# Kernel optimization log

Hardware: AMD Instinct MI355X
Metric: run time of the kernel (lower is better)

The kernel has to match this reference:

```python
import jax, jax.numpy as jnp
import numpy as np

EMBED = 4096
HEADS = 16
HEAD_DIM = EMBED // HEADS  # 256
ROT = 64                   # rotary_dim
B, S = 1, 2048
MASK_VAL = -1.0e9          # masked_bias


def setup_inputs() -> dict:
    key = jax.random.key(0)
    ks = jax.random.split(key, 5)
    sc = 0.02
    return {
        "hidden_states": jax.random.normal(ks[0], (B, S, EMBED), jnp.float32),
        "Wq": jax.random.normal(ks[1], (EMBED, EMBED), jnp.float32) * sc,
        "Wk": jax.random.normal(ks[2], (EMBED, EMBED), jnp.float32) * sc,
        "Wv": jax.random.normal(ks[3], (EMBED, EMBED), jnp.float32) * sc,
        "Wo": jax.random.normal(ks[4], (EMBED, EMBED), jnp.float32) * sc,
    }


def _rotate_every_two(x):
    # interleave: (x0,x1,x2,x3,...) -> (x1,x0,x3,x2,...)  [as written in source]
    r = jnp.stack((x[..., 1::2], x[..., ::2]), axis=-1)
    return r.reshape(x.shape)


def _fixed_pos_embedding(seq_len, rot_dim):
    inv_freq = 1.0 / (10000.0 ** (jnp.arange(0, rot_dim, 2, dtype=jnp.float32) / rot_dim))
    t = jnp.arange(seq_len, dtype=jnp.float32)
    sinusoid = jnp.einsum('i,j->ij', t, inv_freq)  # [S, rot_dim/2]
    return jnp.sin(sinusoid), jnp.cos(sinusoid)


def _apply_rotary(x, sin, cos):
    # x: [B, S, H, ROT]; sin/cos: [S, ROT/2] -> repeat each freq twice along last dim
    sin = jnp.repeat(sin[None, :, None, :], 2, axis=3)
    cos = jnp.repeat(cos[None, :, None, :], 2, axis=3)
    return x * cos + _rotate_every_two(x) * sin


def reference(hidden_states, Wq, Wk, Wv, Wo):
    b, s, e = hidden_states.shape
    q = (hidden_states @ Wq).reshape(b, s, HEADS, HEAD_DIM)
    k = (hidden_states @ Wk).reshape(b, s, HEADS, HEAD_DIM)
    v = (hidden_states @ Wv).reshape(b, s, HEADS, HEAD_DIM)

    sin, cos = _fixed_pos_embedding(s, ROT)
    q = jnp.concatenate([_apply_rotary(q[..., :ROT], sin, cos), q[..., ROT:]], axis=-1)
    k = jnp.concatenate([_apply_rotary(k[..., :ROT], sin, cos), k[..., ROT:]], axis=-1)

    q = q.transpose(0, 2, 1, 3)  # [B,H,S,D]
    k = k.transpose(0, 2, 1, 3)
    v = v.transpose(0, 2, 1, 3)

    logits = jnp.einsum('bhqd,bhkd->bhqk', q, k)  # [B,H,S,S]
    causal = jnp.tril(jnp.ones((s, s), dtype=bool))[None, None]
    # GPT-J quirk: mask applied BEFORE scaling
    logits = jnp.where(causal, logits, MASK_VAL)
    logits = logits / jnp.sqrt(jnp.float32(HEAD_DIM))
    attn = jax.nn.softmax(logits, axis=-1)

    out = jnp.einsum('bhqk,bhkd->bhqd', attn, v)
    out = out.transpose(0, 2, 1, 3).reshape(b, s, e)
    return out @ Wo
```

## Files before the change

kernel.cpp:

```cpp
#include <hip/hip_runtime.h>
#include <hip/hip_bf16.h>
#include <math.h>

#define EMBED 4096
#define SLEN 2048
#define HEADS 16
#define HDIM 256
#define ROT 64

typedef __bf16 bf16;
typedef __attribute__((ext_vector_type(8))) __bf16 bf16x8;
typedef __attribute__((ext_vector_type(4))) float f32x4;

__device__ __forceinline__ void async_copy16(const void* g, void* l) {
  __builtin_amdgcn_global_load_lds((const __attribute__((address_space(1))) void*)g,
                                   (__attribute__((address_space(3))) void*)l,
                                   16, 0, 0);
}

__global__ __launch_bounds__(256) void cast_kernel(const float* __restrict__ in,
                                                   bf16* __restrict__ out, int n4) {
  int i = blockIdx.x * 256 + threadIdx.x;
  if (i >= n4) return;
  float4 v = ((const float4*)in)[i];
  bf16 o[4] __attribute__((aligned(8)));
  o[0] = (bf16)v.x; o[1] = (bf16)v.y; o[2] = (bf16)v.z; o[3] = (bf16)v.w;
  ((ushort4*)out)[i] = *(const ushort4*)o;
}

__global__ __launch_bounds__(256) void transpose_cast(const float* __restrict__ W,
                                                      bf16* __restrict__ Wt) {
  __shared__ bf16 tile[64][65];
  int k0 = blockIdx.y * 64, n0 = blockIdx.x * 64;
  int tr = threadIdx.x >> 4, tc = threadIdx.x & 15;
#pragma unroll
  for (int i = 0; i < 4; i++) {
    int row = tr + i * 16;
    float4 v = *(const float4*)(W + (size_t)(k0 + row) * EMBED + n0 + tc * 4);
    tile[row][tc * 4 + 0] = (bf16)v.x;
    tile[row][tc * 4 + 1] = (bf16)v.y;
    tile[row][tc * 4 + 2] = (bf16)v.z;
    tile[row][tc * 4 + 3] = (bf16)v.w;
  }
  __syncthreads();
#pragma unroll
  for (int i = 0; i < 4; i++) {
    int nl = tr + i * 16;
    bf16 o[4] __attribute__((aligned(8)));
#pragma unroll
    for (int j = 0; j < 4; j++) o[j] = tile[tc * 4 + j][nl];
    *(ushort4*)(Wt + (size_t)(n0 + nl) * EMBED + k0 + tc * 4) = *(const ushort4*)o;
  }
}

template <int MODE>
__global__ __launch_bounds__(512, 1) void gemm_pipe(const bf16* __restrict__ A,
                                                    const bf16* __restrict__ Bt,
                                                    void* __restrict__ Cout,
                                                    int M, int N, int K) {
  constexpr int BM = 128, BN = 256, BK = 64;
  __shared__ __align__(16) bf16 As[3][BM * BK];
  __shared__ __align__(16) bf16 Bs[3][BN * BK];
  int t = threadIdx.x;
  int lane = t & 63, w = t >> 6;
  int c16 = lane & 15, g4 = lane >> 4;
  int wm = w >> 2, wn = w & 3;
  int m0 = blockIdx.y * BM, n0 = blockIdx.x * BN;
  int nt = K / BK;

  f32x4 acc[4][4] = {};

  auto stage = [&](int kt, int slot) {
    const bf16* Asrc = A + (size_t)m0 * K + kt * BK;
    const bf16* Bsrc = Bt + (size_t)n0 * K + kt * BK;
    bf16* Ad = As[slot];
    bf16* Bd = Bs[slot];
#pragma unroll
    for (int i = 0; i < 2; i++) {
      int c = i * 512 + t;
      int row = c >> 3, col8 = c & 7;
      async_copy16(Asrc + (size_t)row * K + ((col8 ^ (row & 7)) * 8), Ad + c * 8);
    }
#pragma unroll
    for (int i = 0; i < 4; i++) {
      int c = i * 512 + t;
      int row = c >> 3, col8 = c & 7;
      async_copy16(Bsrc + (size_t)row * K + ((col8 ^ (row & 7)) * 8), Bd + c * 8);
    }
  };

  stage(0, 0);
  stage(1, 1);
  asm volatile("s_waitcnt vmcnt(6)" ::: "memory");
  __builtin_amdgcn_s_barrier();

  for (int kt = 0; kt < nt; kt++) {
    int slot = kt - (kt / 3) * 3;
    const bf16* Ab = As[slot];
    const bf16* Bb = Bs[slot];

    bf16x8 af[2][4], bfr[2][4];
#pragma unroll
    for (int kk = 0; kk < 2; kk++) {
#pragma unroll
      for (int fm = 0; fm < 4; fm++) {
        int row = wm * 64 + fm * 16 + c16;
        af[kk][fm] = *(const bf16x8*)(Ab + row * BK + (((kk * 4 + g4) ^ (row & 7)) * 8));
      }
#pragma unroll
      for (int fn = 0; fn < 4; fn++) {
        int row = wn * 64 + fn * 16 + c16;
        bfr[kk][fn] = *(const bf16x8*)(Bb + row * BK + (((kk * 4 + g4) ^ (row & 7)) * 8));
      }
    }
    if (kt + 2 < nt) {
      int s2 = (kt + 2) - ((kt + 2) / 3) * 3;
      stage(kt + 2, s2);
    }
    __builtin_amdgcn_s_setprio(1);
#pragma unroll
    for (int kk = 0; kk < 2; kk++)
#pragma unroll
      for (int fm = 0; fm < 4; fm++)
#pragma unroll
        for (int fn = 0; fn < 4; fn++)
          acc[fm][fn] = __builtin_amdgcn_mfma_f32_16x16x32_bf16(af[kk][fm], bfr[kk][fn],
                                                                acc[fm][fn], 0, 0, 0);
    __builtin_amdgcn_s_setprio(0);
    if (kt < nt - 2) {
      asm volatile("s_waitcnt vmcnt(6)" ::: "memory");
      __builtin_amdgcn_s_barrier();
    } else if (kt == nt - 2) {
      asm volatile("s_waitcnt vmcnt(0)" ::: "memory");
      __builtin_amdgcn_s_barrier();
    }
  }

#pragma unroll
  for (int fm = 0; fm < 4; fm++) {
#pragma unroll
    for (int fn = 0; fn < 4; fn++) {
      int col = n0 + wn * 64 + fn * 16 + c16;
#pragma unroll
      for (int r = 0; r < 4; r++) {
        int row = m0 + wm * 64 + fm * 16 + g4 * 4 + r;
        float v = acc[fm][fn][r];
        if (MODE == 1) {
          int d = col & (HDIM - 1);
          if (d < ROT) {
            float pv = __shfl_xor(v, 1);
            int jj = d >> 1;
            float invf = __expf(-0.28782313662425575f * (float)jj);
            float ang = (float)row * invf;
            float sa, ca;
            sincosf(ang, &sa, &ca);
            v = v * ca + pv * sa;
          }
        }
        if (MODE == 3) {
          ((float*)Cout)[(size_t)row * N + col] = v;
        } else if (MODE == 2) {
          ((bf16*)Cout)[(size_t)col * M + row] = (bf16)v;
        } else {
          ((bf16*)Cout)[(size_t)row * N + col] = (bf16)v;
        }
      }
    }
  }
}

__global__ __launch_bounds__(256, 1) void attn_kernel(const bf16* __restrict__ Q,
                                                      const bf16* __restrict__ Kmat,
                                                      const bf16* __restrict__ Vt,
                                                      bf16* __restrict__ O) {
  __shared__ __align__(16) bf16 Ks[2][64 * 256];
  __shared__ __align__(16) bf16 Vs[2][64 * 256];
  __shared__ __align__(16) bf16 Pl[4][16 * 64];
  int t = threadIdx.x, lane = t & 63, w = t >> 6;
  int c16 = lane & 15, g4 = lane >> 4;
  int b = blockIdx.x;
  int h = (b & 7) * 2 + ((b >> 3) & 1);
  int pair = b >> 4;

  for (int pass = 0; pass < 2; ++pass) {
    int qt = pass ? (31 - pair) : pair;
    int q0w = qt * 64 + w * 16;

    bf16x8 qf[8];
    {
      const bf16* qp = Q + (size_t)(q0w + c16) * EMBED + h * HDIM + g4 * 8;
#pragma unroll
      for (int kk = 0; kk < 8; kk++) qf[kk] = *(const bf16x8*)(qp + kk * 32);
    }
    f32x4 acco[16] = {};
    float mrow[4], lrow[4];
#pragma unroll
    for (int r = 0; r < 4; r++) { mrow[r] = -1e30f; lrow[r] = 0.f; }

    __syncthreads();
#pragma unroll
    for (int j = 0; j < 8; j++) {
      int c = j * 256 + w * 64 + lane;
      int row = c >> 5, col8 = c & 31;
      int scol = (col8 ^ (row & 7)) * 8;
      async_copy16(Kmat + (size_t)(0 * 64 + row) * EMBED + h * HDIM + scol,
                   Ks[0] + (size_t)c * 8);
    }
#pragma unroll
    for (int j = 0; j < 8; j++) {
      int c = j * 256 + w * 64 + lane;
      int row = c >> 3, col8 = c & 7;
      int scol = (col8 ^ (row & 7)) * 8;
      async_copy16(Vt + (size_t)(h * HDIM + row) * SLEN + 0 * 64 + scol,
                   Vs[0] + (size_t)c * 8);
    }
    __syncthreads();

    for (int kt = 0; kt <= qt; kt++) {
      int cur = kt & 1;
      if (kt < qt) {
#pragma unroll
        for (int j = 0; j < 8; j++) {
          int c = j * 256 + w * 64 + lane;
          int row = c >> 5, col8 = c & 31;
          int scol = (col8 ^ (row & 7)) * 8;
          async_copy16(Kmat + (size_t)((kt + 1) * 64 + row) * EMBED + h * HDIM + scol,
                       Ks[cur ^ 1] + (size_t)c * 8);
        }
#pragma unroll
        for (int j = 0; j < 8; j++) {
          int c = j * 256 + w * 64 + lane;
          int row = c >> 3, col8 = c & 7;
          int scol = (col8 ^ (row & 7)) * 8;
          async_copy16(Vt + (size_t)(h * HDIM + row) * SLEN + (kt + 1) * 64 + scol,
                       Vs[cur ^ 1] + (size_t)c * 8);
        }
      }
      const bf16* KsB = Ks[cur];
      const bf16* VsB = Vs[cur];

      f32x4 accs[4] = {};
      __builtin_amdgcn_s_setprio(1);
#pragma unroll
      for (int kk = 0; kk < 8; kk++) {
#pragma unroll
        for (int fn = 0; fn < 4; fn++) {
          int r = fn * 16 + c16;
          bf16x8 kf = *(const bf16x8*)(KsB + r * 256 + ((kk * 4 + g4) ^ (c16 & 7)) * 8);
          accs[fn] = __builtin_amdgcn_mfma_f32_16x16x32_bf16(qf[kk], kf, accs[fn], 0, 0, 0);
        }
      }
      __builtin_amdgcn_s_setprio(0);

      float pm[4][4];
      bool diag = (kt == qt);
#pragma unroll
      for (int fn = 0; fn < 4; fn++)
#pragma unroll
        for (int r = 0; r < 4; r++) {
          float s = accs[fn][r] * 0.0625f;
          if (diag) {
            int kg = fn * 16 + c16;
            int qg = w * 16 + g4 * 4 + r;
            if (kg > qg) s = -1e30f;
          }
          pm[fn][r] = s;
        }
      float lmax[4];
#pragma unroll
      for (int r = 0; r < 4; r++)
        lmax[r] = fmaxf(fmaxf(pm[0][r], pm[1][r]), fmaxf(pm[2][r], pm[3][r]));
      bool need = false;
#pragma unroll
      for (int r = 0; r < 4; r++) need = need || (lmax[r] > mrow[r] + 8.0f);
      if (__any(need)) {
#pragma unroll
        for (int r = 0; r < 4; r++) {
          float mx = lmax[r];
#pragma unroll
          for (int off = 1; off < 16; off <<= 1) mx = fmaxf(mx, __shfl_xor(mx, off));
          float mn = fmaxf(mrow[r], mx);
          float sc = __expf(mrow[r] - mn);
          mrow[r] = mn;
          lrow[r] *= sc;
#pragma unroll
          for (int fd = 0; fd < 16; fd++) acco[fd][r] *= sc;
        }
      }
#pragma unroll
      for (int fn = 0; fn < 4; fn++)
#pragma unroll
        for (int r = 0; r < 4; r++) {
          float p = __expf(pm[fn][r] - mrow[r]);
          pm[fn][r] = p;
          lrow[r] += p;
        }
#pragma unroll
      for (int fn = 0; fn < 4; fn++)
#pragma unroll
        for (int r = 0; r < 4; r++) {
          int q = g4 * 4 + r;
          int chunk = (fn * 2 + (c16 >> 3)) ^ (q & 7);
          Pl[w][q * 64 + chunk * 8 + (c16 & 7)] = (bf16)pm[fn][r];
        }
      __builtin_amdgcn_s_setprio(1);
#pragma unroll
      for (int kk2 = 0; kk2 < 2; kk2++) {
        bf16x8 pf = *(const bf16x8*)(&Pl[w][c16 * 64 + ((kk2 * 4 + g4) ^ (c16 & 7)) * 8]);
#pragma unroll
        for (int fd = 0; fd < 16; fd++) {
          int rv = fd * 16 + c16;
          bf16x8 vf = *(const bf16x8*)(VsB + rv * 64 + ((kk2 * 4 + g4) ^ (c16 & 7)) * 8);
          acco[fd] = __builtin_amdgcn_mfma_f32_16x16x32_bf16(pf, vf, acco[fd], 0, 0, 0);
        }
      }
      __builtin_amdgcn_s_setprio(0);
      __syncthreads();
    }
    float inv[4];
#pragma unroll
    for (int r = 0; r < 4; r++) {
      float s = lrow[r];
#pragma unroll
      for (int off = 1; off < 16; off <<= 1) s += __shfl_xor(s, off);
      inv[r] = 1.0f / s;
    }
#pragma unroll
    for (int fd = 0; fd < 16; fd++)
#pragma unroll
      for (int r = 0; r < 4; r++) {
        int qg = q0w + g4 * 4 + r;
        int col = h * HDIM + fd * 16 + c16;
        O[(size_t)qg * EMBED + col] = (bf16)(acco[fd][r] * inv[r]);
      }
  }
}

extern "C" void kernel_launch(void* const* d_in, const int* in_sizes, int n_in,
                              void* d_out, int out_size, void* d_ws, size_t ws_size,
                              hipStream_t stream) {
  const float* hidden = (const float*)d_in[0];
  const float* Wq = (const float*)d_in[1];
  const float* Wk = (const float*)d_in[2];
  const float* Wv = (const float*)d_in[3];
  const float* Wo = (const float*)d_in[4];
  float* out = (float*)d_out;

  char* ws = (char*)d_ws;
  const size_t SZ_H = (size_t)SLEN * EMBED * 2;
  const size_t SZ_W = (size_t)EMBED * EMBED * 2;
  if (ws_size < 5 * SZ_H + SZ_W) return;

  bf16* h_bf = (bf16*)ws;
  bf16* Wt   = (bf16*)(ws + SZ_H);
  bf16* Qb   = (bf16*)(ws + SZ_H + SZ_W);
  bf16* Kb   = (bf16*)(ws + 2 * SZ_H + SZ_W);
  bf16* Vtb  = (bf16*)(ws + 3 * SZ_H + SZ_W);
  bf16* Ob   = (bf16*)(ws + 4 * SZ_H + SZ_W);

  cast_kernel<<<(SLEN * EMBED / 4 + 255) / 256, 256, 0, stream>>>(hidden, h_bf,
                                                                  SLEN * EMBED / 4);

  dim3 tgrid(EMBED / 64, EMBED / 64);
  dim3 ggrid(EMBED / 256, SLEN / 128);

  transpose_cast<<<tgrid, 256, 0, stream>>>(Wq, Wt);
  gemm_pipe<1><<<ggrid, 512, 0, stream>>>(h_bf, Wt, Qb, SLEN, EMBED, EMBED);

  transpose_cast<<<tgrid, 256, 0, stream>>>(Wk, Wt);
  gemm_pipe<1><<<ggrid, 512, 0, stream>>>(h_bf, Wt, Kb, SLEN, EMBED, EMBED);

  transpose_cast<<<tgrid, 256, 0, stream>>>(Wv, Wt);
  gemm_pipe<2><<<ggrid, 512, 0, stream>>>(h_bf, Wt, Vtb, SLEN, EMBED, EMBED);

  attn_kernel<<<dim3(256), 256, 0, stream>>>(Qb, Kb, Vtb, Ob);

  transpose_cast<<<tgrid, 256, 0, stream>>>(Wo, Wt);
  gemm_pipe<3><<<ggrid, 512, 0, stream>>>(Ob, Wt, out, SLEN, EMBED, EMBED);
}
```

Before: 466.7 us.

## Single-buffer K/V tiles in LDS to allow two attention blocks per CU

The attention kernel drops its double-buffered K and V shared-memory tiles for single buffers, roughly halving LDS use, and raises the launch bound to two blocks per CU. The next K tile is now prefetched right after the QK^T MFMAs, and the next V tile right after the PV MFMAs, each behind an extra barrier. The aim is higher occupancy so other blocks hide load latency. The cost is less prefetch overlap inside a block and an extra barrier per iteration. With a grid of about one block per CU, the added occupancy may not be used.

```diff
diff --git a/kernel.cpp b/kernel.cpp
--- a/kernel.cpp
+++ b/kernel.cpp
@@ -169,12 +169,12 @@
   }
 }
 
-__global__ __launch_bounds__(256, 1) void attn_kernel(const bf16* __restrict__ Q,
+__global__ __launch_bounds__(256, 2) void attn_kernel(const bf16* __restrict__ Q,
                                                       const bf16* __restrict__ Kmat,
                                                       const bf16* __restrict__ Vt,
                                                       bf16* __restrict__ O) {
-  __shared__ __align__(16) bf16 Ks[2][64 * 256];
-  __shared__ __align__(16) bf16 Vs[2][64 * 256];
+  __shared__ __align__(16) bf16 Ks[64 * 256];
+  __shared__ __align__(16) bf16 Vs[64 * 256];
   __shared__ __align__(16) bf16 Pl[4][16 * 64];
   int t = threadIdx.x, lane = t & 63, w = t >> 6;
   int c16 = lane & 15, g4 = lane >> 4;
@@ -182,6 +182,27 @@
   int h = (b & 7) * 2 + ((b >> 3) & 1);
   int pair = b >> 4;
 
+  auto stageK = [&](int kt) {
+#pragma unroll
+    for (int j = 0; j < 8; j++) {
+      int c = j * 256 + t;
+      int row = c >> 5, col8 = c & 31;
+      async_copy16(Kmat + (size_t)(kt * 64 + row) * EMBED + h * HDIM +
+                       ((col8 ^ (row & 7)) * 8),
+                   Ks + (size_t)c * 8);
+    }
+  };
+  auto stageV = [&](int kt) {
+#pragma unroll
+    for (int j = 0; j < 8; j++) {
+      int c = j * 256 + t;
+      int row = c >> 3, col8 = c & 7;
+      async_copy16(Vt + (size_t)(h * HDIM + row) * SLEN + kt * 64 +
+                       ((col8 ^ (row & 7)) * 8),
+                   Vs + (size_t)c * 8);
+    }
+  };
+
   for (int pass = 0; pass < 2; ++pass) {
     int qt = pass ? (31 - pair) : pair;
     int q0w = qt * 64 + w * 16;
@@ -198,47 +219,11 @@
     for (int r = 0; r < 4; r++) { mrow[r] = -1e30f; lrow[r] = 0.f; }
 
     __syncthreads();
-#pragma unroll
-    for (int j = 0; j < 8; j++) {
-      int c = j * 256 + w * 64 + lane;
-      int row = c >> 5, col8 = c & 31;
-      int scol = (col8 ^ (row & 7)) * 8;
-      async_copy16(Kmat + (size_t)(0 * 64 + row) * EMBED + h * HDIM + scol,
-                   Ks[0] + (size_t)c * 8);
-    }
-#pragma unroll
-    for (int j = 0; j < 8; j++) {
-      int c = j * 256 + w * 64 + lane;
-      int row = c >> 3, col8 = c & 7;
-      int scol = (col8 ^ (row & 7)) * 8;
-      async_copy16(Vt + (size_t)(h * HDIM + row) * SLEN + 0 * 64 + scol,
-                   Vs[0] + (size_t)c * 8);
-    }
+    stageK(0);
+    stageV(0);
     __syncthreads();
 
     for (int kt = 0; kt <= qt; kt++) {
-      int cur = kt & 1;
-      if (kt < qt) {
-#pragma unroll
-        for (int j = 0; j < 8; j++) {
-          int c = j * 256 + w * 64 + lane;
-          int row = c >> 5, col8 = c & 31;
-          int scol = (col8 ^ (row & 7)) * 8;
-          async_copy16(Kmat + (size_t)((kt + 1) * 64 + row) * EMBED + h * HDIM + scol,
-                       Ks[cur ^ 1] + (size_t)c * 8);
-        }
-#pragma unroll
-        for (int j = 0; j < 8; j++) {
-          int c = j * 256 + w * 64 + lane;
-          int row = c >> 3, col8 = c & 7;
-          int scol = (col8 ^ (row & 7)) * 8;
-          async_copy16(Vt + (size_t)(h * HDIM + row) * SLEN + (kt + 1) * 64 + scol,
-                       Vs[cur ^ 1] + (size_t)c * 8);
-        }
-      }
-      const bf16* KsB = Ks[cur];
-      const bf16* VsB = Vs[cur];
-
       f32x4 accs[4] = {};
       __builtin_amdgcn_s_setprio(1);
 #pragma unroll
@@ -246,11 +231,13 @@
 #pragma unroll
         for (int fn = 0; fn < 4; fn++) {
           int r = fn * 16 + c16;
-          bf16x8 kf = *(const bf16x8*)(KsB + r * 256 + ((kk * 4 + g4) ^ (c16 & 7)) * 8);
+          bf16x8 kf = *(const bf16x8*)(Ks + r * 256 + ((kk * 4 + g4) ^ (c16 & 7)) * 8);
           accs[fn] = __builtin_amdgcn_mfma_f32_16x16x32_bf16(qf[kk], kf, accs[fn], 0, 0, 0);
         }
       }
       __builtin_amdgcn_s_setprio(0);
+      __syncthreads();
+      if (kt < qt) stageK(kt + 1);
 
       float pm[4][4];
       bool diag = (kt == qt);
@@ -310,12 +297,13 @@
 #pragma unroll
         for (int fd = 0; fd < 16; fd++) {
           int rv = fd * 16 + c16;
-          bf16x8 vf = *(const bf16x8*)(VsB + rv * 64 + ((kk2 * 4 + g4) ^ (c16 & 7)) * 8);
+          bf16x8 vf = *(const bf16x8*)(Vs + rv * 64 + ((kk2 * 4 + g4) ^ (c16 & 7)) * 8);
           acco[fd] = __builtin_amdgcn_mfma_f32_16x16x32_bf16(pf, vf, acco[fd], 0, 0, 0);
         }
       }
       __builtin_amdgcn_s_setprio(0);
       __syncthreads();
+      if (kt < qt) stageV(kt + 1);
     }
     float inv[4];
 #pragma unroll
```

New measurement: 458.2 us. About the same (-1.8%).
